# Kernel optimization log

Hardware: AMD Instinct MI355X
Metric: run time of the kernel (lower is better)

The kernel has to match this reference:

```python
import jax, jax.numpy as jnp
import numpy as np

B, S, H, T = 32, 1024, 1024, 256
WINDOW = 2
ITERATIONS = 3


def setup_inputs() -> dict:
    key = jax.random.key(0)
    k1, k2, k3, k4, k5, k6 = jax.random.split(key, 6)
    token_feats = jax.random.normal(k1, (B, S, H), dtype=jnp.float32)
    unary_score = jax.random.normal(k2, (B, S, T), dtype=jnp.float32)
    lengths = jax.random.randint(k3, (B,), S // 2, S + 1)  # in [S/2, S]
    mask = (jnp.arange(S)[None, :] < lengths[:, None]).astype(jnp.float32)
    transitions = jax.random.normal(k4, (WINDOW, T, T), dtype=jnp.float32)
    start_transitions = jax.random.normal(k5, (WINDOW, T), dtype=jnp.float32)
    end_transitions = jax.random.normal(k6, (WINDOW, T), dtype=jnp.float32)
    return {
        "token_feats": token_feats,
        "unary_score": unary_score,
        "mask": mask,
        "transitions": transitions,
        "start_transitions": start_transitions,
        "end_transitions": end_transitions,
        "lengths": lengths,
    }


def reference(token_feats, unary_score, mask, transitions, start_transitions,
              end_transitions, lengths):
    # mask unary (and token_feats, as in original; token_feats is unused in
    # the plain-transitions second-order path)
    unary = unary_score * mask[..., None]        # [B,S,T]
    _ = token_feats * mask[..., None]
    q = unary
    batch_range = jnp.arange(q.shape[0])
    for _it in range(ITERATIONS):
        q = jax.nn.softmax(q, axis=-1)
        left_sum = jnp.zeros_like(q)
        right_sum = jnp.zeros_like(q)
        for j in range(1, WINDOW + 1):
            # message from left neighbor at distance j
            left_sum = left_sum.at[:, j:].add(
                jnp.einsum('nsa,ab->nsb', q[:, :-j], transitions[j - 1]))
            # message from right neighbor at distance j
            right_sum = right_sum.at[:, :-j].add(
                jnp.einsum('nsb,ab->nsa', q[:, j:], transitions[j - 1]))
            # end transitions scatter-add at position lengths - j
            right_sum = right_sum.at[batch_range, lengths - j].add(
                end_transitions[j - 1])
        msg = left_sum + right_sum
        # start transitions on first WINDOW positions (broadcast over batch)
        msg = msg.at[:, 0:WINDOW].add(start_transitions)
        q = unary + msg
        q = q * mask[..., None]
    return q
```

## Files before the change

### kernel.cpp

```cpp
#include <hip/hip_runtime.h>
#include <hip/hip_bf16.h>
#include <cstdint>


typedef __attribute__((ext_vector_type(4))) float f32x4;
typedef __attribute__((ext_vector_type(8))) short bf16x8;

__device__ __forceinline__ void load_lds16(const void* g, void* l) {
    __builtin_amdgcn_global_load_lds(
        (const __attribute__((address_space(1))) void*)g,
        (__attribute__((address_space(3))) void*)l, 16, 0, 0);
}

__device__ __forceinline__ void wct_one(const float* __restrict__ trans,
                                        __hip_bfloat16* __restrict__ wct, int e) {
    int n = e >> 10, k = e & 1023;
    int r = k >> 8, kk = k & 255;
    float v;
    if (r == 0)      v = trans[kk * 256 + n];
    else if (r == 1) v = trans[65536 + kk * 256 + n];
    else if (r == 2) v = trans[n * 256 + kk];
    else             v = trans[65536 + n * 256 + kk];
    wct[n * 1024 + k] = __float2bfloat16(v);
}

__device__ __forceinline__ void guard_one(__hip_bfloat16* Pa, __hip_bfloat16* Pb, int g) {
    __hip_bfloat16* P = (g & 32768) ? Pb : Pa;
    int rem = g & 32767;
    int b = rem >> 10, wr = (rem >> 8) & 3, col = rem & 255;
    int row = b * 1028 + ((wr < 2) ? wr : 1024 + wr);
    P[row * 256 + col] = __float2bfloat16(0.f);
}

__device__ __forceinline__ void softmax0_row(const float* __restrict__ unary,
                                             const int* __restrict__ lengths,
                                             __hip_bfloat16* __restrict__ Pa,
                                             int row, int lane) {
    int b = row >> 10, s = row & 1023;
    float mval = (s < lengths[b]) ? 1.f : 0.f;
    float4 x = *((const float4*)(unary + (size_t)row * 256 + lane * 4));
    x.x *= mval; x.y *= mval; x.z *= mval; x.w *= mval;
    float mx = fmaxf(fmaxf(x.x, x.y), fmaxf(x.z, x.w));
    #pragma unroll
    for (int o = 32; o; o >>= 1) mx = fmaxf(mx, __shfl_xor(mx, o));
    float ea = __expf(x.x - mx), eb = __expf(x.y - mx);
    float ec = __expf(x.z - mx), ed = __expf(x.w - mx);
    float sum = ea + eb + ec + ed;
    #pragma unroll
    for (int o = 32; o; o >>= 1) sum += __shfl_xor(sum, o);
    float inv = 1.0f / sum;
    union { ushort4 u; __hip_bfloat16 h[4]; } o4;
    o4.h[0] = __float2bfloat16(ea * inv);
    o4.h[1] = __float2bfloat16(eb * inv);
    o4.h[2] = __float2bfloat16(ec * inv);
    o4.h[3] = __float2bfloat16(ed * inv);
    *((ushort4*)(Pa + ((size_t)b * 1028 + 2 + s) * 256 + lane * 4)) = o4.u;
}

__global__ __launch_bounds__(256) void prep_softmax0(
    const float* __restrict__ unary, const float* __restrict__ trans,
    const int* __restrict__ lengths,
    __hip_bfloat16* __restrict__ Pa, __hip_bfloat16* __restrict__ Pb,
    __hip_bfloat16* __restrict__ WcT)
{
    int tid = threadIdx.x, lane = tid & 63, wid = tid >> 6;
    int blk = blockIdx.x;
    int e0 = (blk * 256 + tid) * 2;
    wct_one(trans, WcT, e0);
    wct_one(trans, WcT, e0 + 1);
    int idx = blk * 256 + tid;
    if (idx < 65536) guard_one(Pa, Pb, idx);
    for (int q = 0; q < 16; ++q)
        softmax0_row(unary, lengths, Pa, blk * 64 + wid * 16 + q, lane);
}

__global__ __launch_bounds__(512, 4) void mfvi_iter_k(
    const __hip_bfloat16* __restrict__ Pin,
    const __hip_bfloat16* __restrict__ WcT,
    const float* __restrict__ unary, const int* __restrict__ lengths,
    const float* __restrict__ startT, const float* __restrict__ endT,
    __hip_bfloat16* __restrict__ Pout, float* __restrict__ out, int final_it)
{
    __shared__ __hip_bfloat16 Ps[68 * 128];
    __shared__ __hip_bfloat16 Bs[256 * 64];
    __shared__ float redA[256];
    __shared__ float redB[256];

    int tid = threadIdx.x;
    int lane = tid & 63, w = tid >> 6;
    int cn = lane & 15, quad = lane >> 4;
    int wm = (w >> 2) * 32, wn = (w & 3) * 64;
    int nslice = w & 3;
    int tile = blockIdx.x;
    int b = tile >> 4, s0 = (tile & 15) << 6;
    int len = lengths[b];
    const char* Pbase = (const char*)(Pin + ((size_t)b * 1028 + s0) * 256);

    f32x4 acc[2][4] = {};

    int sr = tid >> 3, sc = tid & 7;

    for (int h = 0; h < 2; ++h) {
        #pragma unroll
        for (int t = 0; t < 3; ++t) {
            int c = t * 512 + tid;
            if (t < 2 || tid < 64) {
                int row = c >> 4, ch = c & 15;
                int gch = (ch & ~7) | ((ch ^ row) & 7);
                load_lds16(Pbase + row * 512 + h * 256 + gch * 16,
                           (char*)Ps + c * 16);
            }
        }
        for (int p = 0; p < 8; ++p) {
            int region = p >> 1;
            int delta = (region == 0) ? -1 : (region == 1) ? -2
                      : (region == 2) ?  1 : 2;
            int k0 = region * 256 + h * 128 + (p & 1) * 64;

            #pragma unroll
            for (int c = 0; c < 4; ++c) {
                int n = c * 64 + sr;
                load_lds16((const char*)(WcT + n * 1024 + k0) + ((sc ^ (n & 7)) << 4),
                           (char*)Bs + c * 8192 + tid * 16);
            }
            __syncthreads();

            #pragma unroll
            for (int kk = 0; kk < 2; ++kk) {
                bf16x8 af[2], bfv[4];
                int gcb = (p & 1) * 8 + kk * 4 + quad;
                #pragma unroll
                for (int i = 0; i < 2; ++i) {
                    int r = wm + (i << 4) + cn + delta + 2;
                    int slot = (gcb & ~7) | ((gcb ^ r) & 7);
                    af[i] = *(const bf16x8*)((const char*)Ps + r * 256 + slot * 16);
                }
                int qb = kk * 4 + quad;
                #pragma unroll
                for (int j = 0; j < 4; ++j) {
                    int n = wn + (j << 4) + cn;
                    bfv[j] = *(const bf16x8*)((char*)Bs + n * 128 + ((qb ^ (n & 7)) << 4));
                }
                #pragma unroll
                for (int i = 0; i < 2; ++i)
                    #pragma unroll
                    for (int j = 0; j < 4; ++j)
                        acc[i][j] = __builtin_amdgcn_mfma_f32_16x16x32_bf16(
                            af[i], bfv[j], acc[i][j], 0, 0, 0);
            }
            __syncthreads();
        }
    }

    #pragma unroll
    for (int i = 0; i < 2; ++i)
        #pragma unroll
        for (int j = 0; j < 4; ++j) {
            int n = wn + (j << 4) + cn;
            #pragma unroll
            for (int r = 0; r < 4; ++r) {
                int s = s0 + wm + (i << 4) + (quad << 2) + r;
                float x = acc[i][j][r];
                if (s == 0)       x += startT[n];
                if (s == 1)       x += startT[256 + n];
                if (s == len - 1) x += endT[n];
                if (s == len - 2) x += endT[256 + n];
                long idx = ((long)((b << 10) + s)) * 256 + n;
                x += unary[idx];
                acc[i][j][r] = (s < len) ? x : 0.f;
            }
        }

    if (final_it) {
        #pragma unroll
        for (int i = 0; i < 2; ++i)
            #pragma unroll
            for (int j = 0; j < 4; ++j) {
                int n = wn + (j << 4) + cn;
                #pragma unroll
                for (int r = 0; r < 4; ++r) {
                    int s = s0 + wm + (i << 4) + (quad << 2) + r;
                    out[((long)((b << 10) + s)) * 256 + n] = acc[i][j][r];
                }
            }
        return;
    }

    #pragma unroll
    for (int i = 0; i < 2; ++i)
        #pragma unroll
        for (int r = 0; r < 4; ++r) {
            float m4 = fmaxf(fmaxf(acc[i][0][r], acc[i][1][r]),
                             fmaxf(acc[i][2][r], acc[i][3][r]));
            m4 = fmaxf(m4, __shfl_xor(m4, 1));
            m4 = fmaxf(m4, __shfl_xor(m4, 2));
            m4 = fmaxf(m4, __shfl_xor(m4, 4));
            m4 = fmaxf(m4, __shfl_xor(m4, 8));
            if (cn == 0)
                redA[(nslice << 6) + wm + (i << 4) + (quad << 2) + r] = m4;
        }
    __syncthreads();
    float M[2][4];
    #pragma unroll
    for (int i = 0; i < 2; ++i)
        #pragma unroll
        for (int r = 0; r < 4; ++r) {
            int row = wm + (i << 4) + (quad << 2) + r;
            M[i][r] = fmaxf(fmaxf(redA[row], redA[64 + row]),
                            fmaxf(redA[128 + row], redA[192 + row]));
        }
    #pragma unroll
    for (int i = 0; i < 2; ++i)
        #pragma unroll
        for (int r = 0; r < 4; ++r) {
            float s4 = 0.f;
            #pragma unroll
            for (int j = 0; j < 4; ++j) {
                float e = __expf(acc[i][j][r] - M[i][r]);
                acc[i][j][r] = e;
                s4 += e;
            }
            s4 += __shfl_xor(s4, 1);
            s4 += __shfl_xor(s4, 2);
            s4 += __shfl_xor(s4, 4);
            s4 += __shfl_xor(s4, 8);
            if (cn == 0)
                redB[(nslice << 6) + wm + (i << 4) + (quad << 2) + r] = s4;
        }
    __syncthreads();
    #pragma unroll
    for (int i = 0; i < 2; ++i)
        #pragma unroll
        for (int r = 0; r < 4; ++r) {
            int row = wm + (i << 4) + (quad << 2) + r;
            float inv = 1.0f / (redB[row] + redB[64 + row] +
                                redB[128 + row] + redB[192 + row]);
            int s = s0 + row;
            #pragma unroll
            for (int j = 0; j < 4; ++j) {
                int n = wn + (j << 4) + cn;
                Pout[((size_t)b * 1028 + 2 + s) * 256 + n] =
                    __float2bfloat16(acc[i][j][r] * inv);
            }
        }
}

extern "C" void kernel_launch(void* const* d_in, const int* in_sizes, int n_in,
                              void* d_out, int out_size, void* d_ws, size_t ws_size,
                              hipStream_t stream) {
    const float* unary  = (const float*)d_in[1];
    const float* trans  = (const float*)d_in[3];
    const float* startT = (const float*)d_in[4];
    const float* endT   = (const float*)d_in[5];
    const int*   lens   = (const int*)d_in[6];

    char* ws = (char*)d_ws;
    __hip_bfloat16* Pa  = (__hip_bfloat16*)ws;
    __hip_bfloat16* Pb  = (__hip_bfloat16*)(ws + ((size_t)32 << 20));
    __hip_bfloat16* WcT = (__hip_bfloat16*)(ws + ((size_t)64 << 20));
    float* out = (float*)d_out;

    prep_softmax0<<<dim3(512), dim3(256), 0, stream>>>(unary, trans, lens, Pa, Pb, WcT);
    mfvi_iter_k<<<dim3(512), dim3(512), 0, stream>>>(Pa, WcT, unary, lens, startT, endT, Pb, nullptr, 0);
    mfvi_iter_k<<<dim3(512), dim3(512), 0, stream>>>(Pb, WcT, unary, lens, startT, endT, Pa, nullptr, 0);
    mfvi_iter_k<<<dim3(512), dim3(512), 0, stream>>>(Pa, WcT, unary, lens, startT, endT, nullptr, out, 1);
}
```

Before: 286.9 us.

## Enlarge MFVI iteration tile to 128 rows with double-buffered transition staging

The per-iteration GEMM kernel now processes 128 sequence rows per block (256 blocks instead of 512), so each warp computes a 64x64 output tile and every staged transition slice is reused across twice as many rows. Transition tiles are split into 32-wide K chunks and double-buffered in LDS, with the next chunk's load issued before the current MFMAs so loads overlap compute. The probability tile is restaged in 64-column quarters. The aim is to cut redundant global and LDS traffic for the weight matrix, at the cost of more accumulator registers, lower occupancy, and only 256 blocks, which may underfill the GPU.

```diff
diff --git a/kernel.cpp b/kernel.cpp
--- a/kernel.cpp
+++ b/kernel.cpp
@@ -74,86 +74,103 @@
         softmax0_row(unary, lengths, Pa, blk * 64 + wid * 16 + q, lane);
 }
 
-__global__ __launch_bounds__(512, 4) void mfvi_iter_k(
+__global__ __launch_bounds__(512, 2) void mfvi_iter_k(
     const __hip_bfloat16* __restrict__ Pin,
     const __hip_bfloat16* __restrict__ WcT,
     const float* __restrict__ unary, const int* __restrict__ lengths,
     const float* __restrict__ startT, const float* __restrict__ endT,
     __hip_bfloat16* __restrict__ Pout, float* __restrict__ out, int final_it)
 {
-    __shared__ __hip_bfloat16 Ps[68 * 128];
-    __shared__ __hip_bfloat16 Bs[256 * 64];
-    __shared__ float redA[256];
-    __shared__ float redB[256];
+    __shared__ __hip_bfloat16 Ps[132 * 64];
+    __shared__ __hip_bfloat16 Bs[2][256 * 32];
+    __shared__ float redA[512];
+    __shared__ float redB[512];
 
     int tid = threadIdx.x;
     int lane = tid & 63, w = tid >> 6;
     int cn = lane & 15, quad = lane >> 4;
-    int wm = (w >> 2) * 32, wn = (w & 3) * 64;
+    int wm = (w >> 2) << 6, wn = (w & 3) << 6;
     int nslice = w & 3;
-    int tile = blockIdx.x;
-    int b = tile >> 4, s0 = (tile & 15) << 6;
+    int blk = blockIdx.x;
+    int b = blk >> 3, mt = blk & 7;
+    int s0 = mt << 7;
     int len = lengths[b];
-    const char* Pbase = (const char*)(Pin + ((size_t)b * 1028 + s0) * 256);
-
-    f32x4 acc[2][4] = {};
-
-    int sr = tid >> 3, sc = tid & 7;
-
-    for (int h = 0; h < 2; ++h) {
-        #pragma unroll
-        for (int t = 0; t < 3; ++t) {
-            int c = t * 512 + tid;
-            if (t < 2 || tid < 64) {
-                int row = c >> 4, ch = c & 15;
-                int gch = (ch & ~7) | ((ch ^ row) & 7);
-                load_lds16(Pbase + row * 512 + h * 256 + gch * 16,
-                           (char*)Ps + c * 16);
-            }
-        }
-        for (int p = 0; p < 8; ++p) {
-            int region = p >> 1;
-            int delta = (region == 0) ? -1 : (region == 1) ? -2
-                      : (region == 2) ?  1 : 2;
-            int k0 = region * 256 + h * 128 + (p & 1) * 64;
-
-            #pragma unroll
-            for (int c = 0; c < 4; ++c) {
-                int n = c * 64 + sr;
-                load_lds16((const char*)(WcT + n * 1024 + k0) + ((sc ^ (n & 7)) << 4),
-                           (char*)Bs + c * 8192 + tid * 16);
-            }
-            __syncthreads();
-
-            #pragma unroll
-            for (int kk = 0; kk < 2; ++kk) {
-                bf16x8 af[2], bfv[4];
-                int gcb = (p & 1) * 8 + kk * 4 + quad;
-                #pragma unroll
-                for (int i = 0; i < 2; ++i) {
-                    int r = wm + (i << 4) + cn + delta + 2;
-                    int slot = (gcb & ~7) | ((gcb ^ r) & 7);
-                    af[i] = *(const bf16x8*)((const char*)Ps + r * 256 + slot * 16);
-                }
-                int qb = kk * 4 + quad;
-                #pragma unroll
-                for (int j = 0; j < 4; ++j) {
-                    int n = wn + (j << 4) + cn;
-                    bfv[j] = *(const bf16x8*)((char*)Bs + n * 128 + ((qb ^ (n & 7)) << 4));
-                }
-                #pragma unroll
-                for (int i = 0; i < 2; ++i)
-                    #pragma unroll
-                    for (int j = 0; j < 4; ++j)
-                        acc[i][j] = __builtin_amdgcn_mfma_f32_16x16x32_bf16(
-                            af[i], bfv[j], acc[i][j], 0, 0, 0);
-            }
-            __syncthreads();
+    const char* PbaseB = (const char*)(Pin + ((size_t)b * 1028 + s0) * 256);
+
+    f32x4 acc[4][4] = {};
+
+    auto stagePs = [&](int q) {
+        #pragma unroll
+        for (int t = 0; t < 2; ++t) {
+            int s = t * 512 + tid;
+            int r = s >> 3, ch = s & 7, g = ch ^ (r & 7);
+            load_lds16(PbaseB + r * 512 + q * 128 + g * 16, (char*)Ps + s * 16);
+        }
+        if (tid < 32) {
+            int s = 1024 + tid;
+            int r = s >> 3, ch = s & 7, g = ch ^ (r & 7);
+            load_lds16(PbaseB + r * 512 + q * 128 + g * 16, (char*)Ps + s * 16);
+        }
+    };
+    auto stageBs = [&](int f) {
+        int q = f >> 3, region = (f >> 1) & 3, hs = f & 1;
+        int koff = region * 256 + q * 64 + hs * 32;
+        char* buf = (char*)Bs[f & 1];
+        #pragma unroll
+        for (int c = 0; c < 2; ++c) {
+            int s = c * 512 + tid;
+            int n = s >> 2, ch = s & 3, g = ch ^ (n & 3);
+            load_lds16((const char*)(WcT + n * 1024 + koff) + g * 16, buf + s * 16);
+        }
+    };
+
+    stagePs(0);
+    stageBs(0);
+    __syncthreads();
+
+    for (int f = 0; f < 32; ++f) {
+        int p = f & 7;
+        if (f < 31 && p != 7) stageBs(f + 1);
+        if (f < 31 && p == 7) stageBs(f + 1);
+
+        int region = (f >> 1) & 3, hs = f & 1;
+        int delta = (region == 0) ? -1 : (region == 1) ? -2
+                  : (region == 2) ?  1 : 2;
+        const char* bbuf = (const char*)Bs[f & 1];
+
+        bf16x8 af[4], bfv[4];
+        #pragma unroll
+        for (int i = 0; i < 4; ++i) {
+            int r = wm + (i << 4) + cn + delta + 2;
+            int g = hs * 4 + quad;
+            int slot = g ^ (r & 7);
+            af[i] = *(const bf16x8*)((const char*)Ps + r * 128 + slot * 16);
+        }
+        #pragma unroll
+        for (int j = 0; j < 4; ++j) {
+            int n = wn + (j << 4) + cn;
+            bfv[j] = *(const bf16x8*)(bbuf + n * 64 + ((quad ^ (n & 3)) << 4));
+        }
+        #pragma unroll
+        for (int i = 0; i < 4; ++i)
+            #pragma unroll
+            for (int j = 0; j < 4; ++j)
+                acc[i][j] = __builtin_amdgcn_mfma_f32_16x16x32_bf16(
+                    af[i], bfv[j], acc[i][j], 0, 0, 0);
+
+        if (f < 31) {
+            if (p == 7) {
+                __syncthreads();
+                stagePs((f + 1) >> 3);
+                __syncthreads();
+            } else {
+                __syncthreads();
+            }
         }
     }
 
     #pragma unroll
-    for (int i = 0; i < 2; ++i)
+    for (int i = 0; i < 4; ++i)
         #pragma unroll
         for (int j = 0; j < 4; ++j) {
             int n = wn + (j << 4) + cn;
@@ -173,7 +190,7 @@
 
     if (final_it) {
         #pragma unroll
-        for (int i = 0; i < 2; ++i)
+        for (int i = 0; i < 4; ++i)
             #pragma unroll
             for (int j = 0; j < 4; ++j) {
                 int n = wn + (j << 4) + cn;
@@ -186,8 +203,9 @@
         return;
     }
 
-    #pragma unroll
-    for (int i = 0; i < 2; ++i)
+    __syncthreads();
+    #pragma unroll
+    for (int i = 0; i < 4; ++i)
         #pragma unroll
         for (int r = 0; r < 4; ++r) {
             float m4 = fmaxf(fmaxf(acc[i][0][r], acc[i][1][r]),
@@ -197,20 +215,20 @@
             m4 = fmaxf(m4, __shfl_xor(m4, 4));
             m4 = fmaxf(m4, __shfl_xor(m4, 8));
             if (cn == 0)
-                redA[(nslice << 6) + wm + (i << 4) + (quad << 2) + r] = m4;
-        }
-    __syncthreads();
-    float M[2][4];
-    #pragma unroll
-    for (int i = 0; i < 2; ++i)
+                redA[(nslice << 7) + wm + (i << 4) + (quad << 2) + r] = m4;
+        }
+    __syncthreads();
+    float M[4][4];
+    #pragma unroll
+    for (int i = 0; i < 4; ++i)
         #pragma unroll
         for (int r = 0; r < 4; ++r) {
             int row = wm + (i << 4) + (quad << 2) + r;
-            M[i][r] = fmaxf(fmaxf(redA[row], redA[64 + row]),
-                            fmaxf(redA[128 + row], redA[192 + row]));
-        }
-    #pragma unroll
-    for (int i = 0; i < 2; ++i)
+            M[i][r] = fmaxf(fmaxf(redA[row], redA[128 + row]),
+                            fmaxf(redA[256 + row], redA[384 + row]));
+        }
+    #pragma unroll
+    for (int i = 0; i < 4; ++i)
         #pragma unroll
         for (int r = 0; r < 4; ++r) {
             float s4 = 0.f;
@@ -225,16 +243,16 @@
             s4 += __shfl_xor(s4, 4);
             s4 += __shfl_xor(s4, 8);
             if (cn == 0)
-                redB[(nslice << 6) + wm + (i << 4) + (quad << 2) + r] = s4;
-        }
-    __syncthreads();
-    #pragma unroll
-    for (int i = 0; i < 2; ++i)
+                redB[(nslice << 7) + wm + (i << 4) + (quad << 2) + r] = s4;
+        }
+    __syncthreads();
+    #pragma unroll
+    for (int i = 0; i < 4; ++i)
         #pragma unroll
         for (int r = 0; r < 4; ++r) {
             int row = wm + (i << 4) + (quad << 2) + r;
-            float inv = 1.0f / (redB[row] + redB[64 + row] +
-                                redB[128 + row] + redB[192 + row]);
+            float inv = 1.0f / (redB[row] + redB[128 + row] +
+                                redB[256 + row] + redB[384 + row]);
             int s = s0 + row;
             #pragma unroll
             for (int j = 0; j < 4; ++j) {
@@ -261,7 +279,7 @@
     float* out = (float*)d_out;
 
     prep_softmax0<<<dim3(512), dim3(256), 0, stream>>>(unary, trans, lens, Pa, Pb, WcT);
-    mfvi_iter_k<<<dim3(512), dim3(512), 0, stream>>>(Pa, WcT, unary, lens, startT, endT, Pb, nullptr, 0);
-    mfvi_iter_k<<<dim3(512), dim3(512), 0, stream>>>(Pb, WcT, unary, lens, startT, endT, Pa, nullptr, 0);
-    mfvi_iter_k<<<dim3(512), dim3(512), 0, stream>>>(Pa, WcT, unary, lens, startT, endT, nullptr, out, 1);
-}
+    mfvi_iter_k<<<dim3(256), dim3(512), 0, stream>>>(Pa, WcT, unary, lens, startT, endT, Pb, nullptr, 0);
+    mfvi_iter_k<<<dim3(256), dim3(512), 0, stream>>>(Pb, WcT, unary, lens, startT, endT, Pa, nullptr, 0);
+    mfvi_iter_k<<<dim3(256), dim3(512), 0, stream>>>(Pa, WcT, unary, lens, startT, endT, nullptr, out, 1);
+}
```

New measurement: 303.6 us. 1.06x slower.

## Prepack transition weights as MFMA fragments and stream B from global into registers

Applied to the files above, without the earlier changes.

The prep kernel now writes the bf16 transition matrix in a per-lane MFMA fragment layout, so the iteration kernel can load B operands straight from global/L2 into registers with double-buffered prefetch instead of staging them through LDS. The whole 64x256 P tile (with halo) is loaded into LDS once and stays there, which removes the per-chunk __syncthreads. Each block shrinks to 4 waves, and each wave now owns all 64 rows and a 64-column slice, which doubles the accumulator count per wave. The cost is more register pressure and lower occupancy (launch bounds 256,3), and every B fragment is read from global memory by each block.

```diff
diff --git a/kernel.cpp b/kernel.cpp
--- a/kernel.cpp
+++ b/kernel.cpp
@@ -12,16 +12,25 @@
         (__attribute__((address_space(3))) void*)l, 16, 0, 0);
 }
 
-__device__ __forceinline__ void wct_one(const float* __restrict__ trans,
-                                        __hip_bfloat16* __restrict__ wct, int e) {
-    int n = e >> 10, k = e & 1023;
-    int r = k >> 8, kk = k & 255;
-    float v;
-    if (r == 0)      v = trans[kk * 256 + n];
-    else if (r == 1) v = trans[65536 + kk * 256 + n];
-    else if (r == 2) v = trans[n * 256 + kk];
-    else             v = trans[65536 + n * 256 + kk];
-    wct[n * 1024 + k] = __float2bfloat16(v);
+__device__ __forceinline__ void wfrag_one(const float* __restrict__ trans,
+                                          __hip_bfloat16* __restrict__ wfrag,
+                                          int gid) {
+    int c = gid >> 10, jp = (gid >> 6) & 15, l = gid & 63;
+    int region = c >> 3;
+    int n = jp * 16 + (l & 15);
+    int kr0 = (c & 7) * 32 + (l >> 4) * 8;
+    union { ushort4 u[2]; __hip_bfloat16 h[8]; } o;
+    #pragma unroll
+    for (int e = 0; e < 8; ++e) {
+        int kr = kr0 + e;
+        float v;
+        if (region == 0)      v = trans[kr * 256 + n];
+        else if (region == 1) v = trans[65536 + kr * 256 + n];
+        else if (region == 2) v = trans[n * 256 + kr];
+        else                  v = trans[65536 + n * 256 + kr];
+        o.h[e] = __float2bfloat16(v);
+    }
+    *((uint4*)(wfrag + (size_t)gid * 8)) = *((uint4*)&o);
 }
 
 __device__ __forceinline__ void guard_one(__hip_bfloat16* Pa, __hip_bfloat16* Pb, int g) {
@@ -61,105 +70,95 @@
     const float* __restrict__ unary, const float* __restrict__ trans,
     const int* __restrict__ lengths,
     __hip_bfloat16* __restrict__ Pa, __hip_bfloat16* __restrict__ Pb,
-    __hip_bfloat16* __restrict__ WcT)
+    __hip_bfloat16* __restrict__ Wfrag)
 {
     int tid = threadIdx.x, lane = tid & 63, wid = tid >> 6;
     int blk = blockIdx.x;
-    int e0 = (blk * 256 + tid) * 2;
-    wct_one(trans, WcT, e0);
-    wct_one(trans, WcT, e0 + 1);
     int idx = blk * 256 + tid;
+    if (blk < 128) wfrag_one(trans, Wfrag, idx);
     if (idx < 65536) guard_one(Pa, Pb, idx);
     for (int q = 0; q < 16; ++q)
         softmax0_row(unary, lengths, Pa, blk * 64 + wid * 16 + q, lane);
 }
 
-__global__ __launch_bounds__(512, 4) void mfvi_iter_k(
+__global__ __launch_bounds__(256, 3) void mfvi_iter_k(
     const __hip_bfloat16* __restrict__ Pin,
-    const __hip_bfloat16* __restrict__ WcT,
+    const __hip_bfloat16* __restrict__ Wfrag,
     const float* __restrict__ unary, const int* __restrict__ lengths,
     const float* __restrict__ startT, const float* __restrict__ endT,
     __hip_bfloat16* __restrict__ Pout, float* __restrict__ out, int final_it)
 {
-    __shared__ __hip_bfloat16 Ps[68 * 128];
-    __shared__ __hip_bfloat16 Bs[256 * 64];
+    __shared__ __hip_bfloat16 Ps[68 * 256];
     __shared__ float redA[256];
     __shared__ float redB[256];
 
     int tid = threadIdx.x;
-    int lane = tid & 63, w = tid >> 6;
+    int lane = tid & 63, wid = tid >> 6;
     int cn = lane & 15, quad = lane >> 4;
-    int wm = (w >> 2) * 32, wn = (w & 3) * 64;
-    int nslice = w & 3;
-    int tile = blockIdx.x;
-    int b = tile >> 4, s0 = (tile & 15) << 6;
+    int wn = wid << 6, wq = wid << 2;
+    int blk = blockIdx.x;
+    int b = blk >> 4, s0 = (blk & 15) << 6;
     int len = lengths[b];
-    const char* Pbase = (const char*)(Pin + ((size_t)b * 1028 + s0) * 256);
-
-    f32x4 acc[2][4] = {};
-
-    int sr = tid >> 3, sc = tid & 7;
-
-    for (int h = 0; h < 2; ++h) {
-        #pragma unroll
-        for (int t = 0; t < 3; ++t) {
-            int c = t * 512 + tid;
-            if (t < 2 || tid < 64) {
-                int row = c >> 4, ch = c & 15;
-                int gch = (ch & ~7) | ((ch ^ row) & 7);
-                load_lds16(Pbase + row * 512 + h * 256 + gch * 16,
-                           (char*)Ps + c * 16);
-            }
-        }
-        for (int p = 0; p < 8; ++p) {
-            int region = p >> 1;
-            int delta = (region == 0) ? -1 : (region == 1) ? -2
-                      : (region == 2) ?  1 : 2;
-            int k0 = region * 256 + h * 128 + (p & 1) * 64;
-
-            #pragma unroll
-            for (int c = 0; c < 4; ++c) {
-                int n = c * 64 + sr;
-                load_lds16((const char*)(WcT + n * 1024 + k0) + ((sc ^ (n & 7)) << 4),
-                           (char*)Bs + c * 8192 + tid * 16);
-            }
-            __syncthreads();
-
-            #pragma unroll
-            for (int kk = 0; kk < 2; ++kk) {
-                bf16x8 af[2], bfv[4];
-                int gcb = (p & 1) * 8 + kk * 4 + quad;
-                #pragma unroll
-                for (int i = 0; i < 2; ++i) {
-                    int r = wm + (i << 4) + cn + delta + 2;
-                    int slot = (gcb & ~7) | ((gcb ^ r) & 7);
-                    af[i] = *(const bf16x8*)((const char*)Ps + r * 256 + slot * 16);
-                }
-                int qb = kk * 4 + quad;
-                #pragma unroll
-                for (int j = 0; j < 4; ++j) {
-                    int n = wn + (j << 4) + cn;
-                    bfv[j] = *(const bf16x8*)((char*)Bs + n * 128 + ((qb ^ (n & 7)) << 4));
-                }
-                #pragma unroll
-                for (int i = 0; i < 2; ++i)
-                    #pragma unroll
-                    for (int j = 0; j < 4; ++j)
-                        acc[i][j] = __builtin_amdgcn_mfma_f32_16x16x32_bf16(
-                            af[i], bfv[j], acc[i][j], 0, 0, 0);
-            }
-            __syncthreads();
-        }
-    }
-
-    #pragma unroll
-    for (int i = 0; i < 2; ++i)
+    const char* PbaseB = (const char*)(Pin + ((size_t)b * 1028 + s0) * 256);
+
+    #pragma unroll
+    for (int t = 0; t < 8; ++t) {
+        int cid = t * 256 + tid;
+        int row = cid >> 5, sl = cid & 31;
+        int g = (sl & ~7) | ((sl ^ row) & 7);
+        load_lds16(PbaseB + row * 512 + g * 16, (char*)Ps + cid * 16);
+    }
+    if (tid < 128) {
+        int cid = 2048 + tid;
+        int row = cid >> 5, sl = cid & 31;
+        int g = (sl & ~7) | ((sl ^ row) & 7);
+        load_lds16(PbaseB + row * 512 + g * 16, (char*)Ps + cid * 16);
+    }
+    __syncthreads();
+
+    f32x4 acc[4][4] = {};
+    const bf16x8* Wf = (const bf16x8*)Wfrag;
+
+    bf16x8 bcur[4], bnxt[4];
+    #pragma unroll
+    for (int j = 0; j < 4; ++j)
+        bcur[j] = Wf[(size_t)(wq + j) * 64 + lane];
+
+    #pragma unroll 4
+    for (int c = 0; c < 32; ++c) {
+        if (c < 31) {
+            #pragma unroll
+            for (int j = 0; j < 4; ++j)
+                bnxt[j] = Wf[(size_t)((c + 1) * 16 + wq + j) * 64 + lane];
+        }
+        int region = c >> 3;
+        int delta = ((region & 2) ? 1 : -1) * ((region & 1) + 1);
+        int gch = (c & 7) * 4 + quad;
+        bf16x8 af[4];
+        #pragma unroll
+        for (int i = 0; i < 4; ++i) {
+            int r = (i << 4) + cn + delta + 2;
+            int slot = (gch & ~7) | ((gch ^ r) & 7);
+            af[i] = *(const bf16x8*)((const char*)Ps + r * 512 + slot * 16);
+        }
+        #pragma unroll
+        for (int i = 0; i < 4; ++i)
+            #pragma unroll
+            for (int j = 0; j < 4; ++j)
+                acc[i][j] = __builtin_amdgcn_mfma_f32_16x16x32_bf16(
+                    af[i], bcur[j], acc[i][j], 0, 0, 0);
+        #pragma unroll
+        for (int j = 0; j < 4; ++j) bcur[j] = bnxt[j];
+    }
+
+    #pragma unroll
+    for (int i = 0; i < 4; ++i)
         #pragma unroll
         for (int j = 0; j < 4; ++j) {
             int n = wn + (j << 4) + cn;
             #pragma unroll
             for (int r = 0; r < 4; ++r) {
-                int s = s0 + wm + (i << 4) + (quad << 2) + r;
+                int s = s0 + (i << 4) + (quad << 2) + r;
                 float x = acc[i][j][r];
                 if (s == 0)       x += startT[n];
                 if (s == 1)       x += startT[256 + n];
@@ -173,13 +172,13 @@
 
     if (final_it) {
         #pragma unroll
-        for (int i = 0; i < 2; ++i)
+        for (int i = 0; i < 4; ++i)
             #pragma unroll
             for (int j = 0; j < 4; ++j) {
                 int n = wn + (j << 4) + cn;
                 #pragma unroll
                 for (int r = 0; r < 4; ++r) {
-                    int s = s0 + wm + (i << 4) + (quad << 2) + r;
+                    int s = s0 + (i << 4) + (quad << 2) + r;
                     out[((long)((b << 10) + s)) * 256 + n] = acc[i][j][r];
                 }
             }
@@ -187,7 +186,7 @@
     }
 
     #pragma unroll
-    for (int i = 0; i < 2; ++i)
+    for (int i = 0; i < 4; ++i)
         #pragma unroll
         for (int r = 0; r < 4; ++r) {
             float m4 = fmaxf(fmaxf(acc[i][0][r], acc[i][1][r]),
@@ -196,21 +195,20 @@
             m4 = fmaxf(m4, __shfl_xor(m4, 2));
             m4 = fmaxf(m4, __shfl_xor(m4, 4));
             m4 = fmaxf(m4, __shfl_xor(m4, 8));
-            if (cn == 0)
-                redA[(nslice << 6) + wm + (i << 4) + (quad << 2) + r] = m4;
+            if (cn == 0) redA[(wid << 6) + (i << 4) + (quad << 2) + r] = m4;
         }
     __syncthreads();
-    float M[2][4];
-    #pragma unroll
-    for (int i = 0; i < 2; ++i)
-        #pragma unroll
-        for (int r = 0; r < 4; ++r) {
-            int row = wm + (i << 4) + (quad << 2) + r;
+    float M[4][4];
+    #pragma unroll
+    for (int i = 0; i < 4; ++i)
+        #pragma unroll
+        for (int r = 0; r < 4; ++r) {
+            int row = (i << 4) + (quad << 2) + r;
             M[i][r] = fmaxf(fmaxf(redA[row], redA[64 + row]),
                             fmaxf(redA[128 + row], redA[192 + row]));
         }
     #pragma unroll
-    for (int i = 0; i < 2; ++i)
+    for (int i = 0; i < 4; ++i)
         #pragma unroll
         for (int r = 0; r < 4; ++r) {
             float s4 = 0.f;
@@ -224,15 +222,14 @@
             s4 += __shfl_xor(s4, 2);
             s4 += __shfl_xor(s4, 4);
             s4 += __shfl_xor(s4, 8);
-            if (cn == 0)
-                redB[(nslice << 6) + wm + (i << 4) + (quad << 2) + r] = s4;
+            if (cn == 0) redB[(wid << 6) + (i << 4) + (quad << 2) + r] = s4;
         }
     __syncthreads();
     #pragma unroll
-    for (int i = 0; i < 2; ++i)
-        #pragma unroll
-        for (int r = 0; r < 4; ++r) {
-            int row = wm + (i << 4) + (quad << 2) + r;
+    for (int i = 0; i < 4; ++i)
+        #pragma unroll
+        for (int r = 0; r < 4; ++r) {
+            int row = (i << 4) + (quad << 2) + r;
             float inv = 1.0f / (redB[row] + redB[64 + row] +
                                 redB[128 + row] + redB[192 + row]);
             int s = s0 + row;
@@ -255,13 +252,13 @@
     const int*   lens   = (const int*)d_in[6];
 
     char* ws = (char*)d_ws;
-    __hip_bfloat16* Pa  = (__hip_bfloat16*)ws;
-    __hip_bfloat16* Pb  = (__hip_bfloat16*)(ws + ((size_t)32 << 20));
-    __hip_bfloat16* WcT = (__hip_bfloat16*)(ws + ((size_t)64 << 20));
+    __hip_bfloat16* Pa    = (__hip_bfloat16*)ws;
+    __hip_bfloat16* Pb    = (__hip_bfloat16*)(ws + ((size_t)32 << 20));
+    __hip_bfloat16* Wfrag = (__hip_bfloat16*)(ws + ((size_t)64 << 20));
     float* out = (float*)d_out;
 
-    prep_softmax0<<<dim3(512), dim3(256), 0, stream>>>(unary, trans, lens, Pa, Pb, WcT);
-    mfvi_iter_k<<<dim3(512), dim3(512), 0, stream>>>(Pa, WcT, unary, lens, startT, endT, Pb, nullptr, 0);
-    mfvi_iter_k<<<dim3(512), dim3(512), 0, stream>>>(Pb, WcT, unary, lens, startT, endT, Pa, nullptr, 0);
-    mfvi_iter_k<<<dim3(512), dim3(512), 0, stream>>>(Pa, WcT, unary, lens, startT, endT, nullptr, out, 1);
-}
+    prep_softmax0<<<dim3(512), dim3(256), 0, stream>>>(unary, trans, lens, Pa, Pb, Wfrag);
+    mfvi_iter_k<<<dim3(512), dim3(256), 0, stream>>>(Pa, Wfrag, unary, lens, startT, endT, Pb, nullptr, 0);
+    mfvi_iter_k<<<dim3(512), dim3(256), 0, stream>>>(Pb, Wfrag, unary, lens, startT, endT, Pa, nullptr, 0);
+    mfvi_iter_k<<<dim3(512), dim3(256), 0, stream>>>(Pa, Wfrag, unary, lens, startT, endT, nullptr, out, 1);
+}
```

Result: slower. 294.4 us (+2.6%).
